# Kernel tuning notes

Hardware: AMD Instinct MI355X
Metric: run time of the kernel (lower is better)

The kernel has to match this reference:

```python
import jax, jax.numpy as jnp
import numpy as np

MAXDISP = 128
B, C, H, W = 2, 1, 384, 768
CENSUS_BITS = 24  # original counts bits 0..23 via 24 shift/and/add steps


def setup_inputs() -> dict:
    key = jax.random.key(0)
    k1, k2 = jax.random.split(key)
    image1 = jax.random.randint(k1, (B, C, H, W), 0, 1 << CENSUS_BITS, dtype=jnp.int32)
    image2 = jax.random.randint(k2, (B, C, H, W), 0, 1 << CENSUS_BITS, dtype=jnp.int32)
    scale = jnp.ones((1,), dtype=jnp.float32)  # identity scale (==1), see notes
    return {"image1": image1, "image2": image2, "scale": scale}


def reference(image1, image2, scale):
    b, c, h, w = image1.shape
    d = MAXDISP
    # output[b, d, :, x] = popcount(left[x+d] ^ right[x]) for x < w-d, else 0
    off = jnp.arange(d)[:, None] + jnp.arange(w)[None, :]          # (D, W)
    valid = off < w                                                # (D, W)
    idx = jnp.minimum(off, w - 1)
    left_shift = jnp.take(image1, idx, axis=3)                     # (B, C, H, D, W)
    x = jnp.transpose(left_shift, (0, 3, 1, 2, 4)) ^ image2[:, None]  # (B, D, C, H, W)
    ham = jnp.zeros_like(x)
    for _ in range(CENSUS_BITS):  # vectorized popcount over low 24 bits
        ham = ham + (x & 1)
        x = x >> 1
    ham = jnp.where(valid[None, :, None, None, :], ham, 0)
    ham = ham.reshape(b, d * c, h, w)  # matches torch.cat over d along channel axis
    return ham.astype(jnp.float32) * scale[0]
```

## Files before the change

### kernel.cpp

```cpp
#include <hip/hip_runtime.h>

constexpr int BB = 2;
constexpr int DD = 128;
constexpr int HH = 384;
constexpr int WW = 768;
constexpr int W4 = WW / 4;

__global__ __launch_bounds__(192) void Hamming_34205119545967_kernel(
    const int* __restrict__ img1, const int* __restrict__ img2,
    const float* __restrict__ scale, float* __restrict__ out) {
    const int h = blockIdx.x;
    const int d = blockIdx.y;
    const int b = blockIdx.z;
    const int x4 = threadIdx.x;

    const int4* __restrict__ L4 =
        reinterpret_cast<const int4*>(img1 + ((size_t)b * HH + h) * WW);
    const int4* __restrict__ R4 =
        reinterpret_cast<const int4*>(img2 + ((size_t)b * HH + h) * WW);

    const int4 r = R4[x4];

    const int q  = d >> 2;
    const int rm = d & 3;
    const int ia = min(x4 + q,     W4 - 1);
    const int ib = min(x4 + q + 1, W4 - 1);
    const int4 A = L4[ia];
    const int4 B = L4[ib];

    int w0, w1, w2, w3;
    switch (rm) {
        case 0:  w0 = A.x; w1 = A.y; w2 = A.z; w3 = A.w; break;
        case 1:  w0 = A.y; w1 = A.z; w2 = A.w; w3 = B.x; break;
        case 2:  w0 = A.z; w1 = A.w; w2 = B.x; w3 = B.y; break;
        default: w0 = A.w; w1 = B.x; w2 = B.y; w3 = B.z; break;
    }

    const float s  = scale[0];
    const int  off = (x4 << 2) + d;
    float4 o;
    o.x = (off + 0 < WW) ? (float)__popc(w0 ^ r.x) * s : 0.0f;
    o.y = (off + 1 < WW) ? (float)__popc(w1 ^ r.y) * s : 0.0f;
    o.z = (off + 2 < WW) ? (float)__popc(w2 ^ r.z) * s : 0.0f;
    o.w = (off + 3 < WW) ? (float)__popc(w3 ^ r.w) * s : 0.0f;

    float4* __restrict__ orow =
        reinterpret_cast<float4*>(out + (((size_t)b * DD + d) * HH + h) * WW);
    orow[x4] = o;
}

extern "C" void kernel_launch(void* const* d_in, const int* in_sizes, int n_in,
                              void* d_out, int out_size, void* d_ws, size_t ws_size,
                              hipStream_t stream) {
    const int*   img1  = (const int*)d_in[0];
    const int*   img2  = (const int*)d_in[1];
    const float* scale = (const float*)d_in[2];
    float*       out   = (float*)d_out;

    dim3 grid(HH, DD, BB);
    dim3 block(192);
    Hamming_34205119545967_kernel<<<grid, block, 0, stream>>>(img1, img2, scale, out);
}
```

Measured before the change: 303.8 us.

## Process 32 disparities per block reusing loaded row vectors

Each block now covers a group of 32 disparities instead of one. It loads the right-image row vector once and slides left-image int4 vectors through a register window, so each loaded vector is reused across four shifted disparities. This removes redundant global loads and per-block launch overhead. In exchange the grid has fewer blocks and each thread writes 32 outputs. The kernel is dominated by output writes (about 300MB), so the gain may be limited.

After: 306.9 us. About the same (+1.0%).

```diff
diff --git a/kernel.cpp b/kernel.cpp
--- a/kernel.cpp
+++ b/kernel.cpp
@@ -5,13 +5,15 @@
 constexpr int HH = 384;
 constexpr int WW = 768;
 constexpr int W4 = WW / 4;
+constexpr int DG = 32;
+constexpr int QG = DG / 4;
 
 __global__ __launch_bounds__(192) void Hamming_34205119545967_kernel(
     const int* __restrict__ img1, const int* __restrict__ img2,
     const float* __restrict__ scale, float* __restrict__ out) {
-    const int h = blockIdx.x;
-    const int d = blockIdx.y;
-    const int b = blockIdx.z;
+    const int h  = blockIdx.x;
+    const int dg = blockIdx.y;
+    const int b  = blockIdx.z;
     const int x4 = threadIdx.x;
 
     const int4* __restrict__ L4 =
@@ -19,34 +21,38 @@
     const int4* __restrict__ R4 =
         reinterpret_cast<const int4*>(img2 + ((size_t)b * HH + h) * WW);
 
-    const int4 r = R4[x4];
+    const int4  r = R4[x4];
+    const float s = scale[0];
 
-    const int q  = d >> 2;
-    const int rm = d & 3;
-    const int ia = min(x4 + q,     W4 - 1);
-    const int ib = min(x4 + q + 1, W4 - 1);
-    const int4 A = L4[ia];
-    const int4 B = L4[ib];
+    int q = dg * QG;
+    int4 A = L4[min(x4 + q, W4 - 1)];
 
-    int w0, w1, w2, w3;
-    switch (rm) {
-        case 0:  w0 = A.x; w1 = A.y; w2 = A.z; w3 = A.w; break;
-        case 1:  w0 = A.y; w1 = A.z; w2 = A.w; w3 = B.x; break;
-        case 2:  w0 = A.z; w1 = A.w; w2 = B.x; w3 = B.y; break;
-        default: w0 = A.w; w1 = B.x; w2 = B.y; w3 = B.z; break;
+    const size_t drow = (size_t)HH * W4;
+    float4* __restrict__ obase = reinterpret_cast<float4*>(out) +
+        (((size_t)b * DD + (dg * DG)) * HH + h) * W4 + x4;
+
+#define EMIT(w0, w1, w2, w3, rm)                                       \
+    {                                                                  \
+        const int o_ = off0 + (rm);                                    \
+        float4 o;                                                      \
+        o.x = (o_ + 0 < WW) ? (float)__popc((w0) ^ r.x) * s : 0.0f;    \
+        o.y = (o_ + 1 < WW) ? (float)__popc((w1) ^ r.y) * s : 0.0f;    \
+        o.z = (o_ + 2 < WW) ? (float)__popc((w2) ^ r.z) * s : 0.0f;    \
+        o.w = (o_ + 3 < WW) ? (float)__popc((w3) ^ r.w) * s : 0.0f;    \
+        obase[(size_t)(4 * qq + (rm)) * drow] = o;                     \
     }
 
-    const float s  = scale[0];
-    const int  off = (x4 << 2) + d;
-    float4 o;
-    o.x = (off + 0 < WW) ? (float)__popc(w0 ^ r.x) * s : 0.0f;
-    o.y = (off + 1 < WW) ? (float)__popc(w1 ^ r.y) * s : 0.0f;
-    o.z = (off + 2 < WW) ? (float)__popc(w2 ^ r.z) * s : 0.0f;
-    o.w = (off + 3 < WW) ? (float)__popc(w3 ^ r.w) * s : 0.0f;
-
-    float4* __restrict__ orow =
-        reinterpret_cast<float4*>(out + (((size_t)b * DD + d) * HH + h) * WW);
-    orow[x4] = o;
+#pragma unroll
+    for (int qq = 0; qq < QG; ++qq, ++q) {
+        const int4 Bv = L4[min(x4 + q + 1, W4 - 1)];
+        const int off0 = ((x4 + q) << 2);
+        EMIT(A.x, A.y, A.z, A.w, 0)
+        EMIT(A.y, A.z, A.w, Bv.x, 1)
+        EMIT(A.z, A.w, Bv.x, Bv.y, 2)
+        EMIT(A.w, Bv.x, Bv.y, Bv.z, 3)
+        A = Bv;
+    }
+#undef EMIT
 }
 
 extern "C" void kernel_launch(void* const* d_in, const int* in_sizes, int n_in,
@@ -57,7 +63,7 @@
     const float* scale = (const float*)d_in[2];
     float*       out   = (float*)d_out;
 
-    dim3 grid(HH, DD, BB);
+    dim3 grid(HH, DD / DG, BB);
     dim3 block(192);
     Hamming_34205119545967_kernel<<<grid, block, 0, stream>>>(img1, img2, scale, out);
 }
```
